# Kernel tuning notes

Hardware: AMD Instinct MI355X
Metric: run time of the kernel (lower is better)

Reference implementation:

```python
import jax, jax.numpy as jnp
import numpy as np

N = 1024
H = 1024
B, T = 64, 256


def setup_inputs() -> dict:
    key = jax.random.key(0)
    ks = jax.random.split(key, 12)
    inp = {
        "h_time": jax.random.normal(ks[0], (B, T, H), dtype=jnp.float32),
        "A_pearson": jax.random.uniform(ks[1], (N, N), dtype=jnp.float32),
        "E_dyn": jax.random.normal(ks[2], (N, H), dtype=jnp.float32) * 0.1,
        "alpha_raw": jnp.float32(0.5),
        "tau_raw": jnp.float32(1.0),
        # gate_gen: Linear(H, H//2) -> GELU -> Linear(H//2, N) -> Sigmoid
        "gate_W1": jax.random.normal(ks[3], (H, H // 2), dtype=jnp.float32) * (1.0 / np.sqrt(H)),
        "gate_b1": jnp.zeros((H // 2,), dtype=jnp.float32),
        "gate_W2": jax.random.normal(ks[4], (H // 2, N), dtype=jnp.float32) * (1.0 / np.sqrt(H // 2)),
        "gate_b2": jnp.zeros((N,), dtype=jnp.float32),
        "h2n_W": jax.random.normal(ks[5], (H, N), dtype=jnp.float32) * (1.0 / np.sqrt(H)),
        "h2n_b": jnp.zeros((N,), dtype=jnp.float32),
        "n2h_W": jax.random.normal(ks[6], (N, H), dtype=jnp.float32) * (1.0 / np.sqrt(N)),
        "n2h_b": jnp.zeros((H,), dtype=jnp.float32),
        "ln_w": jnp.ones((H,), dtype=jnp.float32),
        "ln_b": jnp.zeros((H,), dtype=jnp.float32),
    }
    return inp


def _layernorm(x, w, b, eps=1e-5):
    mu = x.mean(-1, keepdims=True)
    var = ((x - mu) ** 2).mean(-1, keepdims=True)
    return (x - mu) * jax.lax.rsqrt(var + eps) * w + b


def reference(h_time, A_pearson, E_dyn, alpha_raw, tau_raw,
              gate_W1, gate_b1, gate_W2, gate_b2,
              h2n_W, h2n_b, n2h_W, n2h_b, ln_w, ln_b):
    tau = jax.nn.softplus(tau_raw) + 1e-6
    alpha = jax.nn.sigmoid(alpha_raw)

    h_mean = h_time.mean(axis=(0, 1))                      # [H]
    E = E_dyn + h_mean[None, :]
    E_cur = E / jnp.maximum(jnp.linalg.norm(E, axis=-1, keepdims=True), 1e-12)  # F.normalize

    A_dyn = jax.nn.relu(E_cur @ E_cur.T)                   # [N,N]
    A_dyn = A_dyn / (A_dyn.sum(axis=-1, keepdims=True) + 1e-6)
    A_dyn = 0.5 * (A_dyn + A_dyn.T)
    A_base = alpha * A_pearson + (1.0 - alpha) * A_dyn

    h_gate = h_time.mean(axis=1)                           # [B,H]
    hid = jax.nn.gelu(h_gate @ gate_W1 + gate_b1, approximate=False)
    gamma = jax.nn.sigmoid(hid @ gate_W2 + gate_b2)        # [B,N]

    # Python loop over batch == row-scaling by mean gate
    A_mix = A_base * gamma.mean(axis=0)[:, None]           # [N,N]

    z_nodes = h_time @ h2n_W + h2n_b                       # [B,T,N]
    z_gcn = jnp.einsum('btn,mn->btm', z_nodes, A_mix)      # z_nodes @ A_mix.T
    msg_h = z_gcn @ n2h_W + n2h_b                          # [B,T,H]

    logits = (A_base @ E_cur) / tau                        # [N,H]
    node_attn = jax.nn.softmax(logits, axis=0)
    global_w = jnp.tanh(node_attn.mean(axis=0))            # [H]

    y = h_time * (1.0 + global_w) + msg_h
    return _layernorm(y, ln_w, ln_b)
```

## Files before the change

### kernel.cpp

```cpp
#include <hip/hip_runtime.h>
#include <math.h>

#define H 1024
#define Nn 1024
#define Bb 64
#define Tt 256
#define BT (Bb * Tt)

typedef unsigned short ushort_t;
typedef __attribute__((ext_vector_type(8))) short bf16x8;
typedef __attribute__((ext_vector_type(4))) float f32x4;


__device__ __forceinline__ ushort_t f2bf(float x) {
    union { float f; unsigned u; } v; v.f = x;
    unsigned r = v.u + 0x7FFFu + ((v.u >> 16) & 1u);
    return (ushort_t)(r >> 16);
}
__device__ __forceinline__ float bf2f(ushort_t h) {
    union { unsigned u; float f; } v; v.u = ((unsigned)h) << 16; return v.f;
}

__device__ __forceinline__ float block_reduce_sum_256(float v) {
    __shared__ float sbuf[4];
    __syncthreads();
    #pragma unroll
    for (int off = 32; off > 0; off >>= 1) v += __shfl_down(v, off, 64);
    int lane = threadIdx.x & 63, w = threadIdx.x >> 6;
    if (lane == 0) sbuf[w] = v;
    __syncthreads();
    if (threadIdx.x == 0) sbuf[0] = sbuf[0] + sbuf[1] + sbuf[2] + sbuf[3];
    __syncthreads();
    return sbuf[0];
}

__global__ void k_stage1(const float* __restrict__ h_time, float* __restrict__ hg_part,
                         ushort_t* __restrict__ ht_bf16, const float* __restrict__ n2h_b,
                         float* __restrict__ rowsumS, float* __restrict__ bias_h,
                         const float* __restrict__ n2h_W, const float* __restrict__ h2n_W,
                         const float* __restrict__ W1, const float* __restrict__ W2,
                         ushort_t* __restrict__ n2hWT_h, ushort_t* __restrict__ n2hWT_l,
                         ushort_t* __restrict__ h2nW_h, ushort_t* __restrict__ h2nW_l,
                         float* __restrict__ W1T, float* __restrict__ W2T) {
    __shared__ float tile[32][33];
    int id = blockIdx.x;
    if (id < 512) {
        int b = id >> 3, z = id & 7;
        int col = threadIdx.x * 4;
        if (b == 0 && z == 0) {
            #pragma unroll
            for (int q = 0; q < 4; ++q) {
                rowsumS[col + q] = 0.f;
                bias_h[col + q] = n2h_b[col + q];
            }
        }
        float4 s4 = {0.f, 0.f, 0.f, 0.f};
        #pragma unroll 4
        for (int t = z * 32; t < z * 32 + 32; ++t) {
            size_t o = ((size_t)b * Tt + t) * H + col;
            float4 v = *(const float4*)&h_time[o];
            s4.x += v.x; s4.y += v.y; s4.z += v.z; s4.w += v.w;
            ushort4 h;
            h.x = f2bf(v.x); h.y = f2bf(v.y); h.z = f2bf(v.z); h.w = f2bf(v.w);
            *(ushort4*)&ht_bf16[o] = h;
        }
        *(float4*)&hg_part[(size_t)(b * 8 + z) * H + col] = s4;
        return;
    }
    int tx = threadIdx.x & 31, ty = threadIdx.x >> 5;
    if (id < 1536) {
        int t = id - 512;
        int i0 = (t >> 5) * 32, j0 = (t & 31) * 32;
        #pragma unroll
        for (int q = 0; q < 4; ++q)
            tile[ty + 8 * q][tx] = n2h_W[(size_t)(i0 + ty + 8 * q) * H + j0 + tx];
        __syncthreads();
        #pragma unroll
        for (int q = 0; q < 4; ++q) {
            float v = tile[tx][ty + 8 * q];
            size_t o = (size_t)(j0 + ty + 8 * q) * Nn + i0 + tx;
            ushort_t hh = f2bf(v);
            n2hWT_h[o] = hh;
            n2hWT_l[o] = f2bf(v - bf2f(hh));
        }
    } else if (id < 2560) {
        size_t idx = (size_t)(id - 1536) * 1024 + threadIdx.x * 4;
        float4 v = *(const float4*)&h2n_W[idx];
        float c[4] = {v.x, v.y, v.z, v.w};
        union { ushort_t u[4]; uint2 w; } ph, pl;
        #pragma unroll
        for (int q = 0; q < 4; ++q) {
            ph.u[q] = f2bf(c[q]);
            pl.u[q] = f2bf(c[q] - bf2f(ph.u[q]));
        }
        *(uint2*)&h2nW_h[idx] = ph.w;
        *(uint2*)&h2nW_l[idx] = pl.w;
    } else if (id < 3072) {
        int t = id - 2560;
        int i0 = (t >> 4) * 32, j0 = (t & 15) * 32;
        #pragma unroll
        for (int q = 0; q < 4; ++q)
            tile[ty + 8 * q][tx] = W1[(size_t)(i0 + ty + 8 * q) * 512 + j0 + tx];
        __syncthreads();
        #pragma unroll
        for (int q = 0; q < 4; ++q)
            W1T[(size_t)(j0 + ty + 8 * q) * 1024 + i0 + tx] = tile[tx][ty + 8 * q];
    } else {
        int t = id - 3072;
        int i0 = (t >> 5) * 32, j0 = (t & 31) * 32;
        #pragma unroll
        for (int q = 0; q < 4; ++q)
            tile[ty + 8 * q][tx] = W2[(size_t)(i0 + ty + 8 * q) * 1024 + j0 + tx];
        __syncthreads();
        #pragma unroll
        for (int q = 0; q < 4; ++q)
            W2T[(size_t)(j0 + ty + 8 * q) * 512 + i0 + tx] = tile[tx][ty + 8 * q];
    }
}

__global__ void k_stage2(const float* __restrict__ hg_part, float* __restrict__ h_gate,
                         float* __restrict__ h_mean) {
    int id = blockIdx.x;
    if (id < 256) {
        int b = id >> 2, cb = id & 3;
        int col = cb * 256 + threadIdx.x;
        float s = 0.f;
        #pragma unroll
        for (int z = 0; z < 8; ++z) s += hg_part[(size_t)(b * 8 + z) * H + col];
        h_gate[b * H + col] = s * (1.0f / Tt);
    } else {
        int h = (id - 256) * 256 + threadIdx.x;
        float s = 0.f;
        for (int r = 0; r < 512; ++r) s += hg_part[(size_t)r * H + h];
        h_mean[h] = s * (1.0f / (Bb * Tt));
    }
}

__global__ __launch_bounds__(256) void k_stage3(
    const float* __restrict__ E_dyn, const float* __restrict__ h_mean,
    ushort_t* __restrict__ E_b,
    const float* __restrict__ h_gate, const float* __restrict__ W1T,
    const float* __restrict__ b1, float* __restrict__ hid) {
    if (blockIdx.x < 1024) {
        int n = blockIdx.x;
        float e[4]; float ss = 0.f;
        #pragma unroll
        for (int q = 0; q < 4; ++q) {
            int h = threadIdx.x + 256 * q;
            e[q] = E_dyn[(size_t)n * H + h] + h_mean[h];
            ss += e[q] * e[q];
        }
        float tot = block_reduce_sum_256(ss);
        float scale = 1.0f / fmaxf(sqrtf(tot), 1e-12f);
        #pragma unroll
        for (int q = 0; q < 4; ++q) {
            int h = threadIdx.x + 256 * q;
            E_b[(size_t)n * H + h] = f2bf(e[q] * scale);
        }
        return;
    }
    int gid = (blockIdx.x - 1024) * 4 + (threadIdx.x >> 6);
    int lane = threadIdx.x & 63;
    int b = gid >> 9, j = gid & 511;
    const float* xr = h_gate + b * H;
    const float* wr = W1T + (size_t)j * H;
    float s = 0.f;
    #pragma unroll
    for (int it = 0; it < 4; ++it) {
        int k = it * 256 + lane * 4;
        float4 x4 = *(const float4*)&xr[k];
        float4 w4 = *(const float4*)&wr[k];
        s += x4.x * w4.x + x4.y * w4.y + x4.z * w4.z + x4.w * w4.w;
    }
    #pragma unroll
    for (int off = 32; off > 0; off >>= 1) s += __shfl_down(s, off, 64);
    if (lane == 0) {
        float a = s + b1[j];
        hid[b * 512 + j] = 0.5f * a * (1.0f + erff(a * 0.70710678118654752f));
    }
}

template <int PASSES, int EPI>
__device__ __forceinline__ void gemm64_body(
    int bx, int by,
    const ushort_t* __restrict__ Ah, const ushort_t* __restrict__ Al,
    const ushort_t* __restrict__ Bh, const ushort_t* __restrict__ Bl,
    ushort_t* __restrict__ O1, ushort_t* __restrict__ O2,
    float* __restrict__ fout, const float* __restrict__ fvec,
    int M, int N, int K) {
    constexpr int NST = (PASSES == 3) ? 4 : 2;
    constexpr int BUFSZ = NST * 64 * 64;
    __shared__ ushort_t sStage[2 * BUFSZ];
    const int tid = threadIdx.x, wave = tid >> 6, lane = tid & 63;
    const int quad = lane >> 4, l16 = lane & 15;
    const int m0 = by * 64, n0 = bx * 64;
    const int wm = (wave >> 1) * 32, wn = (wave & 1) * 32;
    const int sw = (l16 & 7) << 3;

    f32x4 acc[2][2];
    #pragma unroll
    for (int i = 0; i < 2; ++i)
        #pragma unroll
        for (int j = 0; j < 2; ++j)
            acc[i][j] = (f32x4){0.f, 0.f, 0.f, 0.f};

    auto stage = [&](int buf, int k0) {
        ushort_t* sAh = sStage + buf * BUFSZ;
        ushort_t* sBh = sAh + 64 * 64;
        ushort_t* sAl = sAh + 2 * 64 * 64;
        ushort_t* sBl = sAh + 3 * 64 * 64;
        #pragma unroll
        for (int inst = 0; inst < 2; ++inst) {
            const int cbase = (wave * 2 + inst) * 64;
            const int c = cbase + lane;
            const int row = c >> 3;
            const int q = (c & 7) ^ (row & 7);
            const size_t offA = (size_t)(m0 + row) * K + k0 + q * 8;
            const size_t offB = (size_t)(n0 + row) * K + k0 + q * 8;
            __builtin_amdgcn_global_load_lds(
                (const __attribute__((address_space(1))) unsigned int*)(Ah + offA),
                (__attribute__((address_space(3))) unsigned int*)&sAh[cbase * 8], 16, 0, 0);
            __builtin_amdgcn_global_load_lds(
                (const __attribute__((address_space(1))) unsigned int*)(Bh + offB),
                (__attribute__((address_space(3))) unsigned int*)&sBh[cbase * 8], 16, 0, 0);
            if constexpr (PASSES == 3) {
                __builtin_amdgcn_global_load_lds(
                    (const __attribute__((address_space(1))) unsigned int*)(Al + offA),
                    (__attribute__((address_space(3))) unsigned int*)&sAl[cbase * 8], 16, 0, 0);
                __builtin_amdgcn_global_load_lds(
                    (const __attribute__((address_space(1))) unsigned int*)(Bl + offB),
                    (__attribute__((address_space(3))) unsigned int*)&sBl[cbase * 8], 16, 0, 0);
            }
        }
    };

    auto compute = [&](int buf) {
        const ushort_t* sAh = sStage + buf * BUFSZ;
        const ushort_t* sBh = sAh + 64 * 64;
        const ushort_t* sAl = sAh + 2 * 64 * 64;
        const ushort_t* sBl = sAh + 3 * 64 * 64;
        #pragma unroll
        for (int half = 0; half < 2; ++half) {
            bf16x8 fah[2], fbh[2];
            bf16x8 fal[PASSES == 3 ? 2 : 1], fbl[PASSES == 3 ? 2 : 1];
            #pragma unroll
            for (int i = 0; i < 2; ++i) {
                const int ko = ((half * 4 + quad) << 3) ^ sw;
                fah[i] = *(const bf16x8*)&sAh[(wm + i * 16 + l16) * 64 + ko];
                fbh[i] = *(const bf16x8*)&sBh[(wn + i * 16 + l16) * 64 + ko];
                if constexpr (PASSES == 3) {
                    fal[i] = *(const bf16x8*)&sAl[(wm + i * 16 + l16) * 64 + ko];
                    fbl[i] = *(const bf16x8*)&sBl[(wn + i * 16 + l16) * 64 + ko];
                }
            }
            #pragma unroll
            for (int i = 0; i < 2; ++i)
                #pragma unroll
                for (int j = 0; j < 2; ++j) {
                    acc[i][j] = __builtin_amdgcn_mfma_f32_16x16x32_bf16(fah[i], fbh[j], acc[i][j], 0, 0, 0);
                    if constexpr (PASSES == 3) {
                        acc[i][j] = __builtin_amdgcn_mfma_f32_16x16x32_bf16(fah[i], fbl[j], acc[i][j], 0, 0, 0);
                        acc[i][j] = __builtin_amdgcn_mfma_f32_16x16x32_bf16(fal[i], fbh[j], acc[i][j], 0, 0, 0);
                    }
                }
        }
    };

    stage(0, 0);
    __syncthreads();
    int cur = 0;
    for (int k0 = 64; k0 < K; k0 += 64) {
        stage(cur ^ 1, k0);
        compute(cur);
        __syncthreads();
        cur ^= 1;
    }
    compute(cur);

    float fv[2];
    if constexpr (EPI == 2) {
        #pragma unroll
        for (int j = 0; j < 2; ++j) fv[j] = fvec[n0 + wn + j * 16 + l16];
    }
    #pragma unroll
    for (int i = 0; i < 2; ++i)
        #pragma unroll
        for (int r = 0; r < 4; ++r) {
            const int m = m0 + wm + i * 16 + quad * 4 + r;
            float rowacc = 0.f;
            #pragma unroll
            for (int j = 0; j < 2; ++j) {
                const size_t o = (size_t)m * N + n0 + wn + j * 16 + l16;
                float v = acc[i][j][r];
                if constexpr (EPI == 1) {
                    v = fmaxf(v, 0.f);
                    O1[o] = f2bf(v);
                    rowacc += v;
                } else if constexpr (EPI == 2) {
                    ushort_t hh = f2bf(v);
                    O1[o] = hh;
                    O2[o] = f2bf(v - bf2f(hh));
                    rowacc += v * fv[j];
                } else {
                    O1[o] = f2bf(v);
                }
            }
            if constexpr (EPI == 1 || EPI == 2) {
                rowacc += __shfl_xor(rowacc, 1);
                rowacc += __shfl_xor(rowacc, 2);
                rowacc += __shfl_xor(rowacc, 4);
                rowacc += __shfl_xor(rowacc, 8);
                if (l16 == 0) atomicAdd(&fout[m], rowacc);
            }
        }
}

__global__ __launch_bounds__(256) void k_stage4(
    const float* __restrict__ hid, const float* __restrict__ W2T,
    const float* __restrict__ b2, float* __restrict__ gmean,
    const ushort_t* __restrict__ E_b, ushort_t* __restrict__ Sb,
    float* __restrict__ rowsumS) {
    if (blockIdx.x < 256) {
        int n = blockIdx.x * 4 + (threadIdx.x >> 6);
        int lane = threadIdx.x & 63;
        const float* wr = W2T + (size_t)n * 512;
        float4 w0 = *(const float4*)&wr[lane * 4];
        float4 w1 = *(const float4*)&wr[256 + lane * 4];
        float bb = b2[n];
        float acc = 0.f;
        for (int b = 0; b < Bb; ++b) {
            const float* xr = hid + b * 512;
            float4 x0 = *(const float4*)&xr[lane * 4];
            float4 x1 = *(const float4*)&xr[256 + lane * 4];
            float s = x0.x * w0.x + x0.y * w0.y + x0.z * w0.z + x0.w * w0.w
                    + x1.x * w1.x + x1.y * w1.y + x1.z * w1.z + x1.w * w1.w;
            #pragma unroll
            for (int off = 32; off > 0; off >>= 1) s += __shfl_down(s, off, 64);
            if (lane == 0) acc += 1.0f / (1.0f + expf(-(s + bb)));
        }
        if (lane == 0) gmean[n] = acc * (1.0f / Bb);
        return;
    }
    int t = blockIdx.x - 256;
    gemm64_body<1, 1>(t & 15, t >> 4, E_b, nullptr, E_b, nullptr,
                      Sb, nullptr, rowsumS, nullptr, Nn, Nn, H);
}

__global__ void k_amixT(const ushort_t* __restrict__ Sb, const float* __restrict__ A_p,
                        const float* __restrict__ rowsumS, const float* __restrict__ gmean,
                        const float* __restrict__ alpha_raw,
                        ushort_t* __restrict__ Th, ushort_t* __restrict__ Tl) {
    __shared__ float tile[32][33];
    int i0 = blockIdx.y * 32, j0 = blockIdx.x * 32;
    int tx = threadIdx.x & 31, ty = threadIdx.x >> 5;
    float alpha = 1.0f / (1.0f + expf(-alpha_raw[0]));
    #pragma unroll
    for (int q = 0; q < 4; ++q) {
        int i = i0 + ty + 8 * q, j = j0 + tx;
        size_t idx = (size_t)i * Nn + j;
        float s = bf2f(Sb[idx]);
        float ad = 0.5f * s * (1.0f / (rowsumS[i] + 1e-6f) + 1.0f / (rowsumS[j] + 1e-6f));
        tile[ty + 8 * q][tx] = gmean[i] * fmaf(alpha, A_p[idx], (1.0f - alpha) * ad);
    }
    __syncthreads();
    #pragma unroll
    for (int q = 0; q < 4; ++q) {
        float v = tile[tx][ty + 8 * q];
        size_t o = (size_t)(j0 + ty + 8 * q) * Nn + i0 + tx;
        ushort_t hh = f2bf(v);
        Th[o] = hh;
        Tl[o] = f2bf(v - bf2f(hh));
    }
}

__global__ __launch_bounds__(256) void k_c1t(
    const ushort_t* __restrict__ Ah, const ushort_t* __restrict__ Al,
    const ushort_t* __restrict__ Bh, const ushort_t* __restrict__ Bl,
    ushort_t* __restrict__ O1, ushort_t* __restrict__ O2,
    float* __restrict__ fout, const float* __restrict__ fvec) {
    gemm64_body<3, 2>(blockIdx.x & 15, blockIdx.x >> 4, Ah, Al, Bh, Bl, O1, O2, fout, fvec,
                      Nn, Nn, Nn);
}
__global__ __launch_bounds__(256) void k_c2t(
    const ushort_t* __restrict__ Ah, const ushort_t* __restrict__ Al,
    const ushort_t* __restrict__ Bh, const ushort_t* __restrict__ Bl,
    ushort_t* __restrict__ O1) {
    gemm64_body<3, 3>(blockIdx.x & 15, blockIdx.x >> 4, Ah, Al, Bh, Bl, O1, nullptr,
                      nullptr, nullptr, Nn, Nn, Nn);
}

__global__ __launch_bounds__(512, 2) void gemm_big(
    const ushort_t* __restrict__ A, const ushort_t* __restrict__ Bt,
    float* __restrict__ fout, const float* __restrict__ fvec,
    int M, int N, int K) {
    constexpr int BUFSZ = 2 * 256 * 64;
    __shared__ ushort_t sStage[2 * BUFSZ];

    const int tid = threadIdx.x;
    const int wave = tid >> 6, lane = tid & 63;
    const int quad = lane >> 4, l16 = lane & 15;
    const int wr = wave >> 2, wc = wave & 3;
    const int xcd = blockIdx.x & 7, idx = blockIdx.x >> 3;
    const int m0 = (xcd * 8 + (idx >> 2)) * 256;
    const int n0 = (idx & 3) * 256;
    const int wm = wr * 128, wn = wc * 64;
    const int swz = l16 & 7;

    f32x4 acc[8][4];
    #pragma unroll
    for (int i = 0; i < 8; ++i)
        #pragma unroll
        for (int j = 0; j < 4; ++j)
            acc[i][j] = (f32x4){0.f, 0.f, 0.f, 0.f};

    auto stage_half = [&](int buf, int k0, int half) {
        ushort_t* sA = sStage + buf * BUFSZ;
        ushort_t* sB = sA + 256 * 64;
        #pragma unroll
        for (int pass = 0; pass < 2; ++pass) {
            const int c = (half * 2 + pass) * 512 + tid;
            const int row = c >> 3;
            const int q = (c & 7) ^ (row & 7);
            const size_t offA = (size_t)(m0 + row) * K + k0 + q * 8;
            const size_t offB = (size_t)(n0 + row) * K + k0 + q * 8;
            __builtin_amdgcn_global_load_lds(
                (const __attribute__((address_space(1))) unsigned int*)(A + offA),
                (__attribute__((address_space(3))) unsigned int*)&sA[c * 8], 16, 0, 0);
            __builtin_amdgcn_global_load_lds(
                (const __attribute__((address_space(1))) unsigned int*)(Bt + offB),
                (__attribute__((address_space(3))) unsigned int*)&sB[c * 8], 16, 0, 0);
        }
    };

    stage_half(0, 0, 0);
    stage_half(0, 0, 1);
    int buf = 0;
    for (int t = 0; t < 16; ++t) {
        __syncthreads();
        const ushort_t* sA = sStage + buf * BUFSZ;
        const ushort_t* sB = sA + 256 * 64;
        #pragma unroll
        for (int s = 0; s < 2; ++s) {
            if (t + 1 < 16) stage_half(buf ^ 1, (t + 1) * 64, s);
            bf16x8 fb[4], fa[8];
            const int ch = (s * 4 + quad) ^ swz;
            #pragma unroll
            for (int j = 0; j < 4; ++j)
                fb[j] = *(const bf16x8*)&sB[(wn + j * 16 + l16) * 64 + ch * 8];
            #pragma unroll
            for (int i = 0; i < 8; ++i)
                fa[i] = *(const bf16x8*)&sA[(wm + i * 16 + l16) * 64 + ch * 8];
            __builtin_amdgcn_s_barrier();
            asm volatile("s_waitcnt lgkmcnt(0)" ::: "memory");
            __builtin_amdgcn_sched_barrier(0);
            __builtin_amdgcn_s_setprio(1);
            #pragma unroll
            for (int i = 0; i < 8; ++i)
                #pragma unroll
                for (int j = 0; j < 4; ++j)
                    acc[i][j] = __builtin_amdgcn_mfma_f32_16x16x32_bf16(fa[i], fb[j], acc[i][j], 0, 0, 0);
            __builtin_amdgcn_s_setprio(0);
            __builtin_amdgcn_s_barrier();
        }
        buf ^= 1;
    }
    __syncthreads();

    float* Es = (float*)sStage + wave * 4096;
    const float SC = 1.0009765622f;

    #pragma unroll
    for (int pass = 0; pass < 2; ++pass) {
        #pragma unroll
        for (int ii = 0; ii < 4; ++ii) {
            const int i = pass * 4 + ii;
            #pragma unroll
            for (int j = 0; j < 4; ++j)
                #pragma unroll
                for (int r = 0; r < 4; ++r)
                    Es[ii * 1024 + (quad * 4 + r) * 64 + j * 16 + l16] = acc[i][j][r];
        }
        __syncthreads();
        #pragma unroll
        for (int ii = 0; ii < 4; ++ii) {
            #pragma unroll
            for (int it = 0; it < 4; ++it) {
                const int idx2 = it * 64 + lane;
                const int row = idx2 >> 4, f4 = idx2 & 15;
                const int m = m0 + wm + (pass * 4 + ii) * 16 + row;
                const int coln = n0 + wn + f4 * 4;
                float4 v = *(const float4*)&Es[ii * 1024 + row * 64 + f4 * 4];
                float4 b4 = *(const float4*)&fvec[coln];
                ushort4 h4 = *(const ushort4*)&A[(size_t)m * N + coln];
                float4 y;
                y.x = v.x + b4.x + SC * bf2f(h4.x);
                y.y = v.y + b4.y + SC * bf2f(h4.y);
                y.z = v.z + b4.z + SC * bf2f(h4.z);
                y.w = v.w + b4.w + SC * bf2f(h4.w);
                *(float4*)&fout[(size_t)m * N + coln] = y;
            }
        }
        __syncthreads();
    }
}

__global__ __launch_bounds__(256) void k_final_ln(const float* __restrict__ ln_w,
                                                  const float* __restrict__ ln_b,
                                                  float* __restrict__ out) {
    int wave = threadIdx.x >> 6, lane = threadIdx.x & 63;
    size_t row = (size_t)blockIdx.x * 4 + wave;
    float4 v[4];
    float s = 0.f;
    #pragma unroll
    for (int q = 0; q < 4; ++q) {
        v[q] = *(const float4*)&out[row * H + q * 256 + lane * 4];
        s += v[q].x + v[q].y + v[q].z + v[q].w;
    }
    #pragma unroll
    for (int off = 1; off < 64; off <<= 1) s += __shfl_xor(s, off, 64);
    float mu = s * (1.0f / H);
    float ss = 0.f;
    #pragma unroll
    for (int q = 0; q < 4; ++q) {
        v[q].x -= mu; v[q].y -= mu; v[q].z -= mu; v[q].w -= mu;
        ss += v[q].x * v[q].x + v[q].y * v[q].y + v[q].z * v[q].z + v[q].w * v[q].w;
    }
    #pragma unroll
    for (int off = 1; off < 64; off <<= 1) ss += __shfl_xor(ss, off, 64);
    float rstd = rsqrtf(ss * (1.0f / H) + 1e-5f);
    #pragma unroll
    for (int q = 0; q < 4; ++q) {
        int k = q * 256 + lane * 4;
        float4 w4 = *(const float4*)&ln_w[k];
        float4 b4 = *(const float4*)&ln_b[k];
        float4 o;
        o.x = fmaf(v[q].x * rstd, w4.x, b4.x);
        o.y = fmaf(v[q].y * rstd, w4.y, b4.y);
        o.z = fmaf(v[q].z * rstd, w4.z, b4.z);
        o.w = fmaf(v[q].w * rstd, w4.w, b4.w);
        *(float4*)&out[row * H + k] = o;
    }
}


extern "C" void kernel_launch(void* const* d_in, const int* in_sizes, int n_in,
                              void* d_out, int out_size, void* d_ws, size_t ws_size,
                              hipStream_t stream) {
    const float* h_time    = (const float*)d_in[0];
    const float* A_p       = (const float*)d_in[1];
    const float* E_dyn     = (const float*)d_in[2];
    const float* alpha_raw = (const float*)d_in[3];
    const float* gW1   = (const float*)d_in[5];
    const float* gb1   = (const float*)d_in[6];
    const float* gW2   = (const float*)d_in[7];
    const float* gb2   = (const float*)d_in[8];
    const float* h2n_W = (const float*)d_in[9];
    const float* h2n_b = (const float*)d_in[10];
    const float* n2h_W = (const float*)d_in[11];
    const float* n2h_b = (const float*)d_in[12];
    const float* ln_w  = (const float*)d_in[13];
    const float* ln_b  = (const float*)d_in[14];
    float* out = (float*)d_out;

    float* ws = (float*)d_ws;
    float* h_gate  = ws;  ws += Bb * H;
    float* h_mean  = ws;  ws += H;
    float* rowsumS = ws;  ws += Nn;
    float* bias_h  = ws;  ws += H;
    float* hid     = ws;  ws += Bb * 512;
    float* gmean   = ws;  ws += Nn;
    float* W1T     = ws;  ws += 512 * H;
    float* W2T     = ws;  ws += H * 512;
    float* hg_part = ws;  ws += 512 * H;
    ws += 256;
    ushort_t* E_b     = (ushort_t*)ws;  ws += (Nn * H) / 2;
    ushort_t* Sb      = (ushort_t*)ws;  ws += (Nn * Nn) / 2;
    ushort_t* AmixT_h = (ushort_t*)ws;  ws += (Nn * Nn) / 2;
    ushort_t* AmixT_l = (ushort_t*)ws;  ws += (Nn * Nn) / 2;
    ushort_t* n2hWT_h = (ushort_t*)ws;  ws += (Nn * H) / 2;
    ushort_t* n2hWT_l = (ushort_t*)ws;  ws += (Nn * H) / 2;
    ushort_t* h2nW_h  = (ushort_t*)ws;  ws += (H * Nn) / 2;
    ushort_t* h2nW_l  = (ushort_t*)ws;  ws += (H * Nn) / 2;
    ushort_t* C1Th    = (ushort_t*)ws;  ws += (H * Nn) / 2;
    ushort_t* C1Tl    = (ushort_t*)ws;  ws += (H * Nn) / 2;
    ushort_t* C2t     = (ushort_t*)ws;  ws += (H * H) / 2;
    ushort_t* ht      = (ushort_t*)ws;  ws += ((size_t)BT * H) / 2;

    k_stage1<<<3584, 256, 0, stream>>>(h_time, hg_part, ht, n2h_b, rowsumS, bias_h,
                                       n2h_W, h2n_W, gW1, gW2,
                                       n2hWT_h, n2hWT_l, h2nW_h, h2nW_l, W1T, W2T);
    k_stage2<<<260, 256, 0, stream>>>(hg_part, h_gate, h_mean);
    k_stage3<<<9216, 256, 0, stream>>>(E_dyn, h_mean, E_b, h_gate, W1T, gb1, hid);
    k_stage4<<<512, 256, 0, stream>>>(hid, W2T, gb2, gmean, E_b, Sb, rowsumS);
    k_amixT<<<dim3(32, 32), 256, 0, stream>>>(Sb, A_p, rowsumS, gmean, alpha_raw, AmixT_h, AmixT_l);
    k_c1t<<<256, 256, 0, stream>>>(n2hWT_h, n2hWT_l, AmixT_h, AmixT_l, C1Th, C1Tl, bias_h, h2n_b);
    k_c2t<<<256, 256, 0, stream>>>(C1Th, C1Tl, h2nW_h, h2nW_l, C2t);
    gemm_big<<<256, 512, 0, stream>>>(ht, C2t, out, bias_h, BT, H, H);
    k_final_ln<<<4096, 256, 0, stream>>>(ln_w, ln_b, out);
}
```

Measured before the change: 316.4 us.

## Split GEMM k-step into four phases with finer vmcnt waits and barriers

Drops the full __syncthreads at the top of each k-tile. Each k-step now runs as four sub-phases, each covering half of the M fragments. The next tile's global-to-LDS loads are issued in two halves, with a partial vmcnt wait so the current buffer is known ready while the prefetch stays in flight. The aim is to interleave LDS reads, MFMA bursts and global loads more finely and to cut register pressure from holding eight A fragments at once. The cost is extra s_barrier calls per tile and a more fragile dependence on the wait-count accounting.

Measured after the change: 318.6 us. Within noise of the previous version (+0.7%).

```diff
diff --git a/kernel.cpp b/kernel.cpp
--- a/kernel.cpp
+++ b/kernel.cpp
@@ -436,31 +436,50 @@
     stage_half(0, 0, 1);
     int buf = 0;
     for (int t = 0; t < 16; ++t) {
-        __syncthreads();
         const ushort_t* sA = sStage + buf * BUFSZ;
         const ushort_t* sB = sA + 256 * 64;
         #pragma unroll
         for (int s = 0; s < 2; ++s) {
-            if (t + 1 < 16) stage_half(buf ^ 1, (t + 1) * 64, s);
-            bf16x8 fb[4], fa[8];
-            const int ch = (s * 4 + quad) ^ swz;
-            #pragma unroll
-            for (int j = 0; j < 4; ++j)
-                fb[j] = *(const bf16x8*)&sB[(wn + j * 16 + l16) * 64 + ch * 8];
-            #pragma unroll
-            for (int i = 0; i < 8; ++i)
-                fa[i] = *(const bf16x8*)&sA[(wm + i * 16 + l16) * 64 + ch * 8];
-            __builtin_amdgcn_s_barrier();
-            asm volatile("s_waitcnt lgkmcnt(0)" ::: "memory");
-            __builtin_amdgcn_sched_barrier(0);
-            __builtin_amdgcn_s_setprio(1);
-            #pragma unroll
-            for (int i = 0; i < 8; ++i)
+            bf16x8 fb[4];
+            const int ch = ((s * 4 + quad) ^ swz) * 8;
+            #pragma unroll
+            for (int mh = 0; mh < 2; ++mh) {
+                const int ph = s * 2 + mh;
+                if (ph == 0) {
+                    if (t + 1 < 16) {
+                        stage_half(buf ^ 1, (t + 1) * 64, 0);
+                        asm volatile("s_waitcnt vmcnt(4)" ::: "memory");
+                    } else {
+                        asm volatile("s_waitcnt vmcnt(0)" ::: "memory");
+                    }
+                    __builtin_amdgcn_s_barrier();
+                    __builtin_amdgcn_sched_barrier(0);
+                } else if (ph == 1) {
+                    if (t + 1 < 16) stage_half(buf ^ 1, (t + 1) * 64, 1);
+                }
+                if (mh == 0) {
+                    #pragma unroll
+                    for (int j = 0; j < 4; ++j)
+                        fb[j] = *(const bf16x8*)&sB[(wn + j * 16 + l16) * 64 + ch];
+                }
+                bf16x8 fa[4];
                 #pragma unroll
-                for (int j = 0; j < 4; ++j)
-                    acc[i][j] = __builtin_amdgcn_mfma_f32_16x16x32_bf16(fa[i], fb[j], acc[i][j], 0, 0, 0);
-            __builtin_amdgcn_s_setprio(0);
-            __builtin_amdgcn_s_barrier();
+                for (int i = 0; i < 4; ++i)
+                    fa[i] = *(const bf16x8*)&sA[(wm + mh * 64 + i * 16 + l16) * 64 + ch];
+                if (ph != 0) __builtin_amdgcn_s_barrier();
+                asm volatile("s_waitcnt lgkmcnt(0)" ::: "memory");
+                __builtin_amdgcn_sched_barrier(0);
+                __builtin_amdgcn_s_setprio(1);
+                #pragma unroll
+                for (int i = 0; i < 4; ++i)
+                    #pragma unroll
+                    for (int j = 0; j < 4; ++j)
+                        acc[mh * 4 + i][j] =
+                            __builtin_amdgcn_mfma_f32_16x16x32_bf16(fa[i], fb[j], acc[mh * 4 + i][j], 0, 0, 0);
+                __builtin_amdgcn_s_setprio(0);
+                __builtin_amdgcn_s_barrier();
+                __builtin_amdgcn_sched_barrier(0);
+            }
         }
         buf ^= 1;
     }
```

## Fuse final LayerNorm into big GEMM with full-row 64xN tiles

Applied to the files above, without the earlier changes.

Retiles the large GEMM so each 512-thread block computes a 64-row strip across all 1024 output columns. The epilogue can then add the residual and bias and apply LayerNorm in-kernel from an LDS scratch buffer. This drops the separate LayerNorm kernel and its full read and write of the fp32 output. The trade-off is that every block now streams the whole 2 MB B matrix through LDS, which gives much lower arithmetic intensity per tile. It also uses about 136 KB of LDS, so only one block fits per CU, and it runs a simpler double-buffered loop without the earlier priority and barrier scheduling.

Measured after the change: 323.3 us. 1.02x slower.

```diff
diff --git a/kernel.cpp b/kernel.cpp
--- a/kernel.cpp
+++ b/kernel.cpp
@@ -389,156 +389,141 @@
                       nullptr, nullptr, Nn, Nn, Nn);
 }
 
-__global__ __launch_bounds__(512, 2) void gemm_big(
+__global__ __launch_bounds__(512, 2) void gemm_ln(
     const ushort_t* __restrict__ A, const ushort_t* __restrict__ Bt,
-    float* __restrict__ fout, const float* __restrict__ fvec,
-    int M, int N, int K) {
-    constexpr int BUFSZ = 2 * 256 * 64;
+    float* __restrict__ out, const float* __restrict__ fvec,
+    const float* __restrict__ ln_w, const float* __restrict__ ln_b) {
+    constexpr int ABUF = 64 * 32;
+    constexpr int BBUF = 1024 * 32;
+    constexpr int BUFSZ = ABUF + BBUF;
     __shared__ ushort_t sStage[2 * BUFSZ];
 
     const int tid = threadIdx.x;
     const int wave = tid >> 6, lane = tid & 63;
     const int quad = lane >> 4, l16 = lane & 15;
-    const int wr = wave >> 2, wc = wave & 3;
-    const int xcd = blockIdx.x & 7, idx = blockIdx.x >> 3;
-    const int m0 = (xcd * 8 + (idx >> 2)) * 256;
-    const int n0 = (idx & 3) * 256;
-    const int wm = wr * 128, wn = wc * 64;
-    const int swz = l16 & 7;
-
-    f32x4 acc[8][4];
-    #pragma unroll
-    for (int i = 0; i < 8; ++i)
-        #pragma unroll
-        for (int j = 0; j < 4; ++j)
+    const int m0 = blockIdx.x * 64;
+    const int wn = wave * 128;
+
+    f32x4 acc[4][8];
+    #pragma unroll
+    for (int i = 0; i < 4; ++i)
+        #pragma unroll
+        for (int j = 0; j < 8; ++j)
             acc[i][j] = (f32x4){0.f, 0.f, 0.f, 0.f};
 
-    auto stage_half = [&](int buf, int k0, int half) {
+    auto stage = [&](int buf, int k0) {
         ushort_t* sA = sStage + buf * BUFSZ;
-        ushort_t* sB = sA + 256 * 64;
-        #pragma unroll
-        for (int pass = 0; pass < 2; ++pass) {
-            const int c = (half * 2 + pass) * 512 + tid;
-            const int row = c >> 3;
-            const int q = (c & 7) ^ (row & 7);
-            const size_t offA = (size_t)(m0 + row) * K + k0 + q * 8;
-            const size_t offB = (size_t)(n0 + row) * K + k0 + q * 8;
+        ushort_t* sB = sA + ABUF;
+        if (tid < 256) {
+            const int row = tid >> 2;
+            const int q = (tid & 3) ^ (row & 3);
             __builtin_amdgcn_global_load_lds(
-                (const __attribute__((address_space(1))) unsigned int*)(A + offA),
-                (__attribute__((address_space(3))) unsigned int*)&sA[c * 8], 16, 0, 0);
+                (const __attribute__((address_space(1))) unsigned int*)
+                    (A + (size_t)(m0 + row) * H + k0 + q * 8),
+                (__attribute__((address_space(3))) unsigned int*)&sA[tid * 8], 16, 0, 0);
+        }
+        #pragma unroll
+        for (int p = 0; p < 8; ++p) {
+            const int c = p * 512 + tid;
+            const int row = c >> 2;
+            const int q = (c & 3) ^ (row & 3);
             __builtin_amdgcn_global_load_lds(
-                (const __attribute__((address_space(1))) unsigned int*)(Bt + offB),
+                (const __attribute__((address_space(1))) unsigned int*)
+                    (Bt + (size_t)row * H + k0 + q * 8),
                 (__attribute__((address_space(3))) unsigned int*)&sB[c * 8], 16, 0, 0);
         }
     };
 
-    stage_half(0, 0, 0);
-    stage_half(0, 0, 1);
+    auto compute = [&](int buf) {
+        const ushort_t* sA = sStage + buf * BUFSZ;
+        const ushort_t* sB = sA + ABUF;
+        bf16x8 fa[4], fb[8];
+        #pragma unroll
+        for (int i = 0; i < 4; ++i) {
+            const int row = i * 16 + l16;
+            fa[i] = *(const bf16x8*)&sA[row * 32 + (quad ^ (row & 3)) * 8];
+        }
+        #pragma unroll
+        for (int j = 0; j < 8; ++j) {
+            const int row = wn + j * 16 + l16;
+            fb[j] = *(const bf16x8*)&sB[row * 32 + (quad ^ (row & 3)) * 8];
+        }
+        #pragma unroll
+        for (int i = 0; i < 4; ++i)
+            #pragma unroll
+            for (int j = 0; j < 8; ++j)
+                acc[i][j] = __builtin_amdgcn_mfma_f32_16x16x32_bf16(fa[i], fb[j], acc[i][j], 0, 0, 0);
+    };
+
+    stage(0, 0);
+    __syncthreads();
     int buf = 0;
-    for (int t = 0; t < 16; ++t) {
-        __syncthreads();
-        const ushort_t* sA = sStage + buf * BUFSZ;
-        const ushort_t* sB = sA + 256 * 64;
-        #pragma unroll
-        for (int s = 0; s < 2; ++s) {
-            if (t + 1 < 16) stage_half(buf ^ 1, (t + 1) * 64, s);
-            bf16x8 fb[4], fa[8];
-            const int ch = (s * 4 + quad) ^ swz;
-            #pragma unroll
-            for (int j = 0; j < 4; ++j)
-                fb[j] = *(const bf16x8*)&sB[(wn + j * 16 + l16) * 64 + ch * 8];
-            #pragma unroll
-            for (int i = 0; i < 8; ++i)
-                fa[i] = *(const bf16x8*)&sA[(wm + i * 16 + l16) * 64 + ch * 8];
-            __builtin_amdgcn_s_barrier();
-            asm volatile("s_waitcnt lgkmcnt(0)" ::: "memory");
-            __builtin_amdgcn_sched_barrier(0);
-            __builtin_amdgcn_s_setprio(1);
-            #pragma unroll
-            for (int i = 0; i < 8; ++i)
-                #pragma unroll
-                for (int j = 0; j < 4; ++j)
-                    acc[i][j] = __builtin_amdgcn_mfma_f32_16x16x32_bf16(fa[i], fb[j], acc[i][j], 0, 0, 0);
-            __builtin_amdgcn_s_setprio(0);
-            __builtin_amdgcn_s_barrier();
-        }
+    for (int t = 0; t < 32; ++t) {
+        if (t + 1 < 32) stage(buf ^ 1, (t + 1) * 32);
+        compute(buf);
+        __syncthreads();
         buf ^= 1;
     }
-    __syncthreads();
-
-    float* Es = (float*)sStage + wave * 4096;
+
     const float SC = 1.0009765622f;
-
-    #pragma unroll
-    for (int pass = 0; pass < 2; ++pass) {
-        #pragma unroll
-        for (int ii = 0; ii < 4; ++ii) {
-            const int i = pass * 4 + ii;
-            #pragma unroll
-            for (int j = 0; j < 4; ++j)
+    float* ySc = (float*)sStage;
+
+    #pragma unroll
+    for (int p = 0; p < 2; ++p) {
+        #pragma unroll
+        for (int ii = 0; ii < 2; ++ii) {
+            const int i = 2 * p + ii;
+            #pragma unroll
+            for (int j = 0; j < 8; ++j)
                 #pragma unroll
                 for (int r = 0; r < 4; ++r)
-                    Es[ii * 1024 + (quad * 4 + r) * 64 + j * 16 + l16] = acc[i][j][r];
-        }
-        __syncthreads();
-        #pragma unroll
-        for (int ii = 0; ii < 4; ++ii) {
-            #pragma unroll
-            for (int it = 0; it < 4; ++it) {
-                const int idx2 = it * 64 + lane;
-                const int row = idx2 >> 4, f4 = idx2 & 15;
-                const int m = m0 + wm + (pass * 4 + ii) * 16 + row;
-                const int coln = n0 + wn + f4 * 4;
-                float4 v = *(const float4*)&Es[ii * 1024 + row * 64 + f4 * 4];
-                float4 b4 = *(const float4*)&fvec[coln];
-                ushort4 h4 = *(const ushort4*)&A[(size_t)m * N + coln];
-                float4 y;
-                y.x = v.x + b4.x + SC * bf2f(h4.x);
-                y.y = v.y + b4.y + SC * bf2f(h4.y);
-                y.z = v.z + b4.z + SC * bf2f(h4.z);
-                y.w = v.w + b4.w + SC * bf2f(h4.w);
-                *(float4*)&fout[(size_t)m * N + coln] = y;
-            }
-        }
-        __syncthreads();
-    }
-}
-
-__global__ __launch_bounds__(256) void k_final_ln(const float* __restrict__ ln_w,
-                                                  const float* __restrict__ ln_b,
-                                                  float* __restrict__ out) {
-    int wave = threadIdx.x >> 6, lane = threadIdx.x & 63;
-    size_t row = (size_t)blockIdx.x * 4 + wave;
-    float4 v[4];
-    float s = 0.f;
-    #pragma unroll
-    for (int q = 0; q < 4; ++q) {
-        v[q] = *(const float4*)&out[row * H + q * 256 + lane * 4];
-        s += v[q].x + v[q].y + v[q].z + v[q].w;
-    }
-    #pragma unroll
-    for (int off = 1; off < 64; off <<= 1) s += __shfl_xor(s, off, 64);
-    float mu = s * (1.0f / H);
-    float ss = 0.f;
-    #pragma unroll
-    for (int q = 0; q < 4; ++q) {
-        v[q].x -= mu; v[q].y -= mu; v[q].z -= mu; v[q].w -= mu;
-        ss += v[q].x * v[q].x + v[q].y * v[q].y + v[q].z * v[q].z + v[q].w * v[q].w;
-    }
-    #pragma unroll
-    for (int off = 1; off < 64; off <<= 1) ss += __shfl_xor(ss, off, 64);
-    float rstd = rsqrtf(ss * (1.0f / H) + 1e-5f);
-    #pragma unroll
-    for (int q = 0; q < 4; ++q) {
-        int k = q * 256 + lane * 4;
-        float4 w4 = *(const float4*)&ln_w[k];
-        float4 b4 = *(const float4*)&ln_b[k];
-        float4 o;
-        o.x = fmaf(v[q].x * rstd, w4.x, b4.x);
-        o.y = fmaf(v[q].y * rstd, w4.y, b4.y);
-        o.z = fmaf(v[q].z * rstd, w4.z, b4.z);
-        o.w = fmaf(v[q].w * rstd, w4.w, b4.w);
-        *(float4*)&out[row * H + k] = o;
+                    ySc[(ii * 16 + quad * 4 + r) * 1028 + wn + j * 16 + l16] = acc[i][j][r];
+        }
+        __syncthreads();
+        #pragma unroll
+        for (int rr = 0; rr < 4; ++rr) {
+            const int lr = wave * 4 + rr;
+            const int m = m0 + p * 32 + lr;
+            float4 y[4];
+            float s = 0.f;
+            #pragma unroll
+            for (int q = 0; q < 4; ++q) {
+                const int cb = q * 256 + lane * 4;
+                float4 v = *(const float4*)&ySc[lr * 1028 + cb];
+                float4 b4 = *(const float4*)&fvec[cb];
+                ushort4 h4 = *(const ushort4*)&A[(size_t)m * H + cb];
+                y[q].x = v.x + b4.x + SC * bf2f(h4.x);
+                y[q].y = v.y + b4.y + SC * bf2f(h4.y);
+                y[q].z = v.z + b4.z + SC * bf2f(h4.z);
+                y[q].w = v.w + b4.w + SC * bf2f(h4.w);
+                s += y[q].x + y[q].y + y[q].z + y[q].w;
+            }
+            #pragma unroll
+            for (int off = 1; off < 64; off <<= 1) s += __shfl_xor(s, off, 64);
+            float mu = s * (1.0f / H);
+            float sq = 0.f;
+            #pragma unroll
+            for (int q = 0; q < 4; ++q) {
+                y[q].x -= mu; y[q].y -= mu; y[q].z -= mu; y[q].w -= mu;
+                sq += y[q].x * y[q].x + y[q].y * y[q].y + y[q].z * y[q].z + y[q].w * y[q].w;
+            }
+            #pragma unroll
+            for (int off = 1; off < 64; off <<= 1) sq += __shfl_xor(sq, off, 64);
+            float rstd = rsqrtf(sq * (1.0f / H) + 1e-5f);
+            #pragma unroll
+            for (int q = 0; q < 4; ++q) {
+                const int cb = q * 256 + lane * 4;
+                float4 w4 = *(const float4*)&ln_w[cb];
+                float4 g4 = *(const float4*)&ln_b[cb];
+                float4 o;
+                o.x = fmaf(y[q].x * rstd, w4.x, g4.x);
+                o.y = fmaf(y[q].y * rstd, w4.y, g4.y);
+                o.z = fmaf(y[q].z * rstd, w4.z, g4.z);
+                o.w = fmaf(y[q].w * rstd, w4.w, g4.w);
+                *(float4*)&out[(size_t)m * H + cb] = o;
+            }
+        }
+        __syncthreads();
     }
 }
 
@@ -595,6 +580,5 @@
     k_amixT<<<dim3(32, 32), 256, 0, stream>>>(Sb, A_p, rowsumS, gmean, alpha_raw, AmixT_h, AmixT_l);
     k_c1t<<<256, 256, 0, stream>>>(n2hWT_h, n2hWT_l, AmixT_h, AmixT_l, C1Th, C1Tl, bias_h, h2n_b);
     k_c2t<<<256, 256, 0, stream>>>(C1Th, C1Tl, h2nW_h, h2nW_l, C2t);
-    gemm_big<<<256, 512, 0, stream>>>(ht, C2t, out, bias_h, BT, H, H);
-    k_final_ln<<<4096, 256, 0, stream>>>(ln_w, ln_b, out);
-}
+    gemm_ln<<<256, 512, 0, stream>>>(ht, C2t, out, bias_h, ln_w, ln_b);
+}
```
